# Kernel tuning notes

Hardware: AMD Instinct MI355X
Metric: run time of the kernel (lower is better)

Reference implementation:

```python
import jax, jax.numpy as jnp
import numpy as np

B, T, NB, D, E = 2, 4096, 4, 512, 4096
TEMP = 1.0
CAP_F = 1.5
NOISE_KEY = 42


def setup_inputs() -> dict:
    key = jax.random.key(0)
    k1, k2 = jax.random.split(key)
    x = jax.random.normal(k1, (B, T, NB * D), dtype=jnp.float32)
    # Tied weights: embedding_table[i].weight is embedding_decoder[i].weight, shape [E, D] per block
    W = jax.random.normal(k2, (NB, E, D), dtype=jnp.float32) * 0.02
    return {"x": x, "W": W}


def reference(x, W):
    Bv, Tv, _ = x.shape
    xb = x.reshape(Bv, Tv, NB, D)
    expert_capacity = int(Bv * Tv / E * CAP_F)  # = 3 here
    # per-block decoder logits: [B, T, NB, E]
    dist_logits = jnp.einsum('btnd,ned->btne', xb, W)
    # noise = 1 - temperature * rand_like(logits)
    noise = 1.0 - TEMP * jax.random.uniform(jax.random.key(NOISE_KEY), dist_logits.shape, dtype=dist_logits.dtype)
    noisy = dist_logits * noise
    # top-k over the token axis T (dim=1 in torch) per (b, block, element)
    nt = noisy.transpose(0, 2, 3, 1)  # [B, NB, E, T]
    _, topk_idx = jax.lax.top_k(nt, expert_capacity)  # [B, NB, E, k]
    mask = jnp.zeros(nt.shape, dtype=bool)
    bI = jnp.arange(Bv)[:, None, None, None]
    nI = jnp.arange(NB)[None, :, None, None]
    eI = jnp.arange(E)[None, None, :, None]
    mask = mask.at[bI, nI, eI, topk_idx].set(True)
    maskf = mask.transpose(0, 3, 1, 2).astype(noisy.dtype)  # [B, T, NB, E]
    # argmax over codebook dim of masked noisy logits
    decoded_indices = jnp.argmax(maskf * noisy, axis=-1)  # [B, T, NB]
    # embedding gather with tied table W[n]: [B, T, NB, D]
    latents = jax.vmap(lambda w, i: w[i], in_axes=(0, 2), out_axes=2)(W, decoded_indices)
    decoded_latents = latents.reshape(Bv, Tv, NB * D)  # cat along dim=2
    return decoded_indices, decoded_latents, dist_logits
```

## Files before the change

### kernel.cpp

```cpp
#include <hip/hip_runtime.h>
#include <stdint.h>

#define B_     2
#define T_     4096
#define NB_    4
#define D_     512
#define E_     4096
#define NE_    16384
#define HALF_  67108864u
#define SLOTS_ 32768
#define XN8_   2097152
#define WN8_   1048576
#define MT_    32
#define RECN_  (64 * NE_)

typedef unsigned long long u64;
typedef uint32_t u32;
typedef uint16_t u16;
typedef _Float16 f16x8 __attribute__((ext_vector_type(8)));
typedef float    f32x4 __attribute__((ext_vector_type(4)));

__device__ __forceinline__ u32 rotl32(u32 x, int r) { return __builtin_rotateleft32(x, r); }

__device__ __forceinline__ void tf_0_42(u32 x0, u32 x1, u32 &o0, u32 &o1) {
  const u32 ks0 = 0u, ks1 = 42u, ks2 = 0x1BD11BDAu ^ 0u ^ 42u;
  x0 += ks0; x1 += ks1;
#define TFR(r) { x0 += x1; x1 = rotl32(x1, (r)); x1 ^= x0; }
  TFR(13) TFR(15) TFR(26) TFR(6)
  x0 += ks1; x1 += ks2 + 1u;
  TFR(17) TFR(29) TFR(16) TFR(24)
  x0 += ks2; x1 += ks0 + 2u;
  TFR(13) TFR(15) TFR(26) TFR(6)
  x0 += ks0; x1 += ks1 + 3u;
  TFR(17) TFR(29) TFR(16) TFR(24)
  x0 += ks1; x1 += ks2 + 4u;
  TFR(13) TFR(15) TFR(26) TFR(6)
  x0 += ks2; x1 += ks0 + 5u;
#undef TFR
  o0 = x0; o1 = x1;
}

__device__ __forceinline__ float noise_at(u32 i) {
  u32 o0, o1; tf_0_42(0u, i, o0, o1);
  u32 bits = o0 ^ o1;
  float f = __uint_as_float((bits >> 9) | 0x3F800000u);
  return 2.0f - f;
}

__device__ __forceinline__ u32 map_f32(float v) {
  u32 u = __float_as_uint(v);
  u32 s = (u32)((int)u >> 31);
  return u ^ (s | 0x80000000u);
}

__device__ __forceinline__ void merge3(u64 &a0, u64 &a1, u64 &a2,
                                       u64 b0, u64 b1, u64 b2) {
  u64 o0, o1, o2;
  if (a0 >= b0) {
    o0 = a0;
    if (a1 >= b0) { o1 = a1; o2 = (a2 >= b0) ? a2 : b0; }
    else          { o1 = b0; o2 = (a1 >= b1) ? a1 : b1; }
  } else {
    o0 = b0;
    if (b1 >= a0) { o1 = b1; o2 = (b2 >= a0) ? b2 : a0; }
    else          { o1 = a0; o2 = (b1 >= a1) ? b1 : a1; }
  }
  a0 = o0; a1 = o1; a2 = o2;
}

#define BASE_KEY 0x80000000FFFFFFFFull
#define SCALE_   2048.0f
#define INV_SC   (1.0f / 4194304.0f)

__global__ __launch_bounds__(256) void init_keys(u64* __restrict__ keys,
                                                 u32* __restrict__ thr) {
  int i = blockIdx.x * 256 + threadIdx.x;
  keys[i] = BASE_KEY;
  thr[i]  = 0u;
}

__device__ __forceinline__ void split8v(const float4 a0, const float4 a1, f16x8 &hi, f16x8 &lo) {
  float fv[8] = {a0.x, a0.y, a0.z, a0.w, a1.x, a1.y, a1.z, a1.w};
#pragma unroll
  for (int j = 0; j < 8; ++j) {
    float f = fv[j] * SCALE_;
    _Float16 h = (_Float16)f;
    hi[j] = h;
    lo[j] = (_Float16)(f - (float)h);
  }
}

__global__ __launch_bounds__(256) void presplit(const float* __restrict__ x,
                                                const float* __restrict__ W,
                                                f16x8* __restrict__ xh, f16x8* __restrict__ xl,
                                                f16x8* __restrict__ wh, f16x8* __restrict__ wl) {
  size_t g = (size_t)blockIdx.x * 256 + threadIdx.x;
  const float4* src;
  f16x8 *dh, *dl;
  size_t off;
  if (g < XN8_) { src = (const float4*)x; dh = xh; dl = xl; off = g; }
  else          { src = (const float4*)W; dh = wh; dl = wl; off = g - XN8_; }
  float4 a0 = src[off * 2], a1 = src[off * 2 + 1];
  f16x8 hi, lo;
  split8v(a0, a1, hi, lo);
  dh[off] = hi; dl[off] = lo;
}

#define BM 128
#define BN 128

__global__ __launch_bounds__(256) void gemm_presample(const f16x8* __restrict__ xh,
                                                      const f16x8* __restrict__ xl,
                                                      const f16x8* __restrict__ wh,
                                                      const f16x8* __restrict__ wl,
                                                      u32* __restrict__ thrbuf) {
  __shared__ f16x8 lds_raw[2048];
  f16x8* AhV = lds_raw;
  f16x8* AlV = lds_raw + 512;
  f16x8* BhV = lds_raw + 1024;
  f16x8* BlV = lds_raw + 1536;

  const int id = blockIdx.x;
  const int e0 = (id & 31) * BN;
  const int n  = (id >> 5) & 3;
  const int b  = id >> 7;

  const int tid  = threadIdx.x;
  const int lane = tid & 63;
  const int wid  = tid >> 6;
  const int wr   = wid >> 1;
  const int wc   = wid & 1;
  const int lm   = lane & 15;
  const int lk   = lane >> 4;

  f32x4 acc[4][4];
#pragma unroll
  for (int i = 0; i < 4; ++i)
#pragma unroll
    for (int j = 0; j < 4; ++j) acc[i][j] = (f32x4){0.f, 0.f, 0.f, 0.f};

  for (int k0 = 0; k0 < D_ / 8; k0 += 4) {
#pragma unroll
    for (int l = 0; l < 2; ++l) {
      int aid = tid + l * 256;
      int r   = aid >> 2;
      int ko  = aid & 3;
      int ps  = ko ^ ((r >> 1) & 3);
      size_t gA = ((size_t)(b * T_ + 32 * r) * NB_ + n) * (D_ / 8) + k0 + ko;
      AhV[r * 4 + ps] = xh[gA];
      AlV[r * 4 + ps] = xl[gA];
      size_t gB = ((size_t)n * E_ + e0 + r) * (D_ / 8) + k0 + ko;
      BhV[r * 4 + ps] = wh[gB];
      BlV[r * 4 + ps] = wl[gB];
    }
    __syncthreads();

    f16x8 bh[4], bl[4];
#pragma unroll
    for (int fn = 0; fn < 4; ++fn) {
      int row = wc * 64 + fn * 16 + lm;
      int ps  = lk ^ ((row >> 1) & 3);
      bh[fn] = BhV[row * 4 + ps];
      bl[fn] = BlV[row * 4 + ps];
    }
#pragma unroll
    for (int fm = 0; fm < 4; ++fm) {
      int row = wr * 64 + fm * 16 + lm;
      int ps  = lk ^ ((row >> 1) & 3);
      f16x8 ah = AhV[row * 4 + ps];
      f16x8 al = AlV[row * 4 + ps];
#pragma unroll
      for (int fn = 0; fn < 4; ++fn) {
        acc[fm][fn] = __builtin_amdgcn_mfma_f32_16x16x32_f16(ah, bh[fn], acc[fm][fn], 0, 0, 0);
        acc[fm][fn] = __builtin_amdgcn_mfma_f32_16x16x32_f16(ah, bl[fn], acc[fm][fn], 0, 0, 0);
        acc[fm][fn] = __builtin_amdgcn_mfma_f32_16x16x32_f16(al, bh[fn], acc[fm][fn], 0, 0, 0);
      }
    }
    __syncthreads();
  }
  u64* ldsK = (u64*)lds_raw;

#pragma unroll
  for (int fn = 0; fn < 4; ++fn) {
    const int e  = e0 + wc * 64 + fn * 16 + lm;
    const int ne = n * E_ + e;
    u32 v0 = 0, v1 = 0, v2 = 0;
    u32 tt0 = 0, tt1 = 0, tt2 = 0;
    const u32 ibase = (u32)b * HALF_ + (u32)ne;
#pragma unroll
    for (int fm = 0; fm < 4; ++fm) {
#pragma unroll
      for (int r = 0; r < 4; ++r) {
        const u32 t = 32u * (u32)(wr * 64 + fm * 16 + lk * 4 + r);
        float lg = acc[fm][fn][r] * INV_SC;
        u32 mu = __float_as_uint(fmaxf(lg, 0.0f)) | 0x80000000u;
        if (mu > v2) {
          float y = lg * noise_at(ibase + t * (u32)NE_);
          u32 mv = map_f32(y);
          bool g0 = mv > v0, g1 = mv > v1, g2 = mv > v2;
          v2  = g1 ? v1  : (g2 ? mv : v2);
          tt2 = g1 ? tt1 : (g2 ? t  : tt2);
          v1  = g0 ? v0  : (g1 ? mv : v1);
          tt1 = g0 ? tt0 : (g1 ? t  : tt1);
          v0  = g0 ? mv  : v0;
          tt0 = g0 ? t   : tt0;
        }
      }
    }
    u64 K0 = ((u64)v0 << 32) | (u64)(0xFFFFFFFFu - tt0);
    u64 K1 = ((u64)v1 << 32) | (u64)(0xFFFFFFFFu - tt1);
    u64 K2 = ((u64)v2 << 32) | (u64)(0xFFFFFFFFu - tt2);
    u64 p0 = __shfl_xor(K0, 16), p1 = __shfl_xor(K1, 16), p2 = __shfl_xor(K2, 16);
    merge3(K0, K1, K2, p0, p1, p2);
    p0 = __shfl_xor(K0, 32); p1 = __shfl_xor(K1, 32); p2 = __shfl_xor(K2, 32);
    merge3(K0, K1, K2, p0, p1, p2);
    if (lk == 0) {
      int c = fn * 16 + lm;
      ldsK[(wid * 64 + c) * 3 + 0] = K0;
      ldsK[(wid * 64 + c) * 3 + 1] = K1;
      ldsK[(wid * 64 + c) * 3 + 2] = K2;
    }
  }
  __syncthreads();
  if (wid < 2) {
    int c = lane;
    u64 A0 = ldsK[(wid * 64 + c) * 3 + 0];
    u64 A1 = ldsK[(wid * 64 + c) * 3 + 1];
    u64 A2 = ldsK[(wid * 64 + c) * 3 + 2];
    merge3(A0, A1, A2,
           ldsK[((wid + 2) * 64 + c) * 3 + 0],
           ldsK[((wid + 2) * 64 + c) * 3 + 1],
           ldsK[((wid + 2) * 64 + c) * 3 + 2]);
    int eg = e0 + wid * 64 + c;
    thrbuf[(size_t)b * NE_ + (size_t)n * E_ + eg] = (u32)(A2 >> 32);
  }
}

__global__ __launch_bounds__(256) void gemm_fused(const f16x8* __restrict__ xh,
                                                  const f16x8* __restrict__ xl,
                                                  const f16x8* __restrict__ wh,
                                                  const f16x8* __restrict__ wl,
                                                  float* __restrict__ logits,
                                                  u64* __restrict__ k0g,
                                                  u64* __restrict__ k1g,
                                                  u64* __restrict__ k2g,
                                                  u32* __restrict__ thrbuf) {
  __shared__ f16x8 lds_raw[2048];
  f16x8* AhV = lds_raw;
  f16x8* AlV = lds_raw + 512;
  f16x8* BhV = lds_raw + 1024;
  f16x8* BlV = lds_raw + 1536;

  const int id = blockIdx.x;
  const int e0 = (id & 31) * BN;
  const int mt = (id >> 5) & 63;
  const int n  = id >> 11;
  const int m0 = mt * BM;

  const int tid  = threadIdx.x;
  const int lane = tid & 63;
  const int wid  = tid >> 6;
  const int wr   = wid >> 1;
  const int wc   = wid & 1;
  const int lm   = lane & 15;
  const int lk   = lane >> 4;

  f32x4 acc[4][4];
#pragma unroll
  for (int i = 0; i < 4; ++i)
#pragma unroll
    for (int j = 0; j < 4; ++j) acc[i][j] = (f32x4){0.f, 0.f, 0.f, 0.f};

  for (int k0 = 0; k0 < D_ / 8; k0 += 4) {
#pragma unroll
    for (int l = 0; l < 2; ++l) {
      int aid = tid + l * 256;
      int r   = aid >> 2;
      int ko  = aid & 3;
      int ps  = ko ^ ((r >> 1) & 3);
      size_t gA = ((size_t)(m0 + r) * NB_ + n) * (D_ / 8) + k0 + ko;
      AhV[r * 4 + ps] = xh[gA];
      AlV[r * 4 + ps] = xl[gA];
      size_t gB = ((size_t)n * E_ + e0 + r) * (D_ / 8) + k0 + ko;
      BhV[r * 4 + ps] = wh[gB];
      BlV[r * 4 + ps] = wl[gB];
    }
    __syncthreads();

    f16x8 bh[4], bl[4];
#pragma unroll
    for (int fn = 0; fn < 4; ++fn) {
      int row = wc * 64 + fn * 16 + lm;
      int ps  = lk ^ ((row >> 1) & 3);
      bh[fn] = BhV[row * 4 + ps];
      bl[fn] = BlV[row * 4 + ps];
    }
#pragma unroll
    for (int fm = 0; fm < 4; ++fm) {
      int row = wr * 64 + fm * 16 + lm;
      int ps  = lk ^ ((row >> 1) & 3);
      f16x8 ah = AhV[row * 4 + ps];
      f16x8 al = AlV[row * 4 + ps];
#pragma unroll
      for (int fn = 0; fn < 4; ++fn) {
        acc[fm][fn] = __builtin_amdgcn_mfma_f32_16x16x32_f16(ah, bh[fn], acc[fm][fn], 0, 0, 0);
        acc[fm][fn] = __builtin_amdgcn_mfma_f32_16x16x32_f16(ah, bl[fn], acc[fm][fn], 0, 0, 0);
        acc[fm][fn] = __builtin_amdgcn_mfma_f32_16x16x32_f16(al, bh[fn], acc[fm][fn], 0, 0, 0);
      }
    }
    __syncthreads();
  }
  float* lgbuf = (float*)lds_raw;
  u16*   tbuf  = (u16*)((char*)lds_raw + 16384);
  u64*   ldsK  = (u64*)((char*)lds_raw + 24576);

  const int b     = m0 >> 12;
  const int mbase = m0 & (T_ - 1);
  const int mtile = mbase >> 7;

#pragma unroll
  for (int fm = 0; fm < 4; ++fm) {
#pragma unroll
    for (int r = 0; r < 4; ++r) {
      int m = m0 + wr * 64 + fm * 16 + lk * 4 + r;
      float* row = logits + ((size_t)m * NB_ + n) * E_ + e0 + wc * 64 + lm;
#pragma unroll
      for (int fn = 0; fn < 4; ++fn) row[fn * 16] = acc[fm][fn][r] * INV_SC;
    }
  }

#pragma unroll
  for (int fn = 0; fn < 4; ++fn) {
    const int e  = e0 + wc * 64 + fn * 16 + lm;
    const int ne = n * E_ + e;
    const u32 thrv = thrbuf[(size_t)b * NE_ + ne];

    int cnt = 0;
#pragma unroll
    for (int fm = 0; fm < 4; ++fm) {
#pragma unroll
      for (int r = 0; r < 4; ++r) {
        float lg = acc[fm][fn][r] * INV_SC;
        u32 mu = __float_as_uint(fmaxf(lg, 0.0f)) | 0x80000000u;
        if (mu >= thrv) {
          lgbuf[cnt * 256 + tid] = lg;
          tbuf [cnt * 256 + tid] = (u16)(mbase + wr * 64 + fm * 16 + lk * 4 + r);
          ++cnt;
        }
      }
    }

    u32 v0 = 0, v1 = 0, v2 = 0;
    u32 tt0 = 0, tt1 = 0, tt2 = 0;
    const u32 ibase = (u32)b * HALF_ + (u32)ne;
    for (int k = 0; k < cnt; ++k) {
      float lg = lgbuf[k * 256 + tid];
      u32 t    = (u32)tbuf[k * 256 + tid];
      float y  = lg * noise_at(ibase + t * (u32)NE_);
      u32 mv = map_f32(y);
      bool g0 = mv > v0, g1 = mv > v1, g2 = mv > v2;
      v2  = g1 ? v1  : (g2 ? mv : v2);
      tt2 = g1 ? tt1 : (g2 ? t  : tt2);
      v1  = g0 ? v0  : (g1 ? mv : v1);
      tt1 = g0 ? tt0 : (g1 ? t  : tt1);
      v0  = g0 ? mv  : v0;
      tt0 = g0 ? t   : tt0;
    }

    u64 K0 = ((u64)v0 << 32) | (u64)(0xFFFFFFFFu - tt0);
    u64 K1 = ((u64)v1 << 32) | (u64)(0xFFFFFFFFu - tt1);
    u64 K2 = ((u64)v2 << 32) | (u64)(0xFFFFFFFFu - tt2);
    u64 p0 = __shfl_xor(K0, 16), p1 = __shfl_xor(K1, 16), p2 = __shfl_xor(K2, 16);
    merge3(K0, K1, K2, p0, p1, p2);
    p0 = __shfl_xor(K0, 32); p1 = __shfl_xor(K1, 32); p2 = __shfl_xor(K2, 32);
    merge3(K0, K1, K2, p0, p1, p2);
    if (lk == 0) {
      int c = fn * 16 + lm;
      ldsK[(wid * 64 + c) * 3 + 0] = K0;
      ldsK[(wid * 64 + c) * 3 + 1] = K1;
      ldsK[(wid * 64 + c) * 3 + 2] = K2;
    }
  }
  __syncthreads();
  if (wid < 2) {
    int c = lane;
    u64 A0 = ldsK[(wid * 64 + c) * 3 + 0];
    u64 A1 = ldsK[(wid * 64 + c) * 3 + 1];
    u64 A2 = ldsK[(wid * 64 + c) * 3 + 2];
    u64 C0 = ldsK[((wid + 2) * 64 + c) * 3 + 0];
    u64 C1 = ldsK[((wid + 2) * 64 + c) * 3 + 1];
    u64 C2 = ldsK[((wid + 2) * 64 + c) * 3 + 2];
    merge3(A0, A1, A2, C0, C1, C2);
    int eg = e0 + wid * 64 + c;
    size_t R = (size_t)(mtile * 2 + b) * NE_ + (size_t)n * E_ + eg;
    k0g[R] = A0; k1g[R] = A1; k2g[R] = A2;
    atomicMax(&thrbuf[(size_t)b * NE_ + (size_t)n * E_ + eg], (u32)(A2 >> 32));
  }
}

__global__ __launch_bounds__(256) void merge_scatter2(const u64* __restrict__ k0g,
                                                      const u64* __restrict__ k1g,
                                                      const u64* __restrict__ k2g,
                                                      u64* __restrict__ keys) {
  int gid2 = blockIdx.x * 256 + threadIdx.x;
  int b  = gid2 >> 14;
  int ne = gid2 & (NE_ - 1);

  u64 K0 = 0, K1 = 0, K2 = 0;
  for (int mt = 0; mt < MT_; ++mt) {
    size_t R = (size_t)(mt * 2 + b) * NE_ + ne;
    merge3(K0, K1, K2, k0g[R], k1g[R], k2g[R]);
  }

  int n = ne >> 12;
  u32 e = (u32)(ne & (E_ - 1));
  u64 elo = (u64)(0xFFFFFFFFu - e);
  u32 t0 = 0xFFFFFFFFu - (u32)K0;
  u32 t1 = 0xFFFFFFFFu - (u32)K1;
  u32 t2 = 0xFFFFFFFFu - (u32)K2;
  atomicMax(&keys[((size_t)b * T_ + t0) * NB_ + n], (K0 & 0xFFFFFFFF00000000ull) | elo);
  atomicMax(&keys[((size_t)b * T_ + t1) * NB_ + n], (K1 & 0xFFFFFFFF00000000ull) | elo);
  atomicMax(&keys[((size_t)b * T_ + t2) * NB_ + n], (K2 & 0xFFFFFFFF00000000ull) | elo);
}

__device__ __forceinline__ void split8(const float* __restrict__ p, f16x8 &hi, f16x8 &lo) {
  float4 a0 = *(const float4*)p;
  float4 a1 = *(const float4*)(p + 4);
  split8v(a0, a1, hi, lo);
}

__global__ __launch_bounds__(256) void gemm_logits_fb(const float* __restrict__ x,
                                                      const float* __restrict__ W,
                                                      float* __restrict__ logits) {
  __shared__ f16x8 AhV[128 * 4];
  __shared__ f16x8 AlV[128 * 4];
  __shared__ f16x8 BhV[128 * 4];
  __shared__ f16x8 BlV[128 * 4];

  const int n  = blockIdx.z;
  const int m0 = blockIdx.y * BM;
  const int e0 = blockIdx.x * BN;
  const int tid  = threadIdx.x;
  const int lane = tid & 63;
  const int wid  = tid >> 6;
  const int wr   = wid >> 1;
  const int wc   = wid & 1;
  const int lm   = lane & 15;
  const int lk   = lane >> 4;

  const float* Abase = x + ((size_t)m0 * NB_ + n) * D_;
  const float* Bbase = W + ((size_t)n * E_ + e0) * D_;

  f32x4 acc[4][4];
#pragma unroll
  for (int i = 0; i < 4; ++i)
#pragma unroll
    for (int j = 0; j < 4; ++j) acc[i][j] = (f32x4){0.f, 0.f, 0.f, 0.f};

  for (int k0 = 0; k0 < D_; k0 += 32) {
#pragma unroll
    for (int l = 0; l < 2; ++l) {
      int aid = tid + l * 256;
      int r   = aid >> 2;
      int ko  = aid & 3;
      int ps  = ko ^ ((r >> 1) & 3);
      f16x8 hi, lo;
      split8(Abase + (size_t)r * (NB_ * D_) + k0 + ko * 8, hi, lo);
      AhV[r * 4 + ps] = hi; AlV[r * 4 + ps] = lo;
      split8(Bbase + (size_t)r * D_ + k0 + ko * 8, hi, lo);
      BhV[r * 4 + ps] = hi; BlV[r * 4 + ps] = lo;
    }
    __syncthreads();

    f16x8 bh[4], bl[4];
#pragma unroll
    for (int fn = 0; fn < 4; ++fn) {
      int row = wc * 64 + fn * 16 + lm;
      int ps  = lk ^ ((row >> 1) & 3);
      bh[fn] = BhV[row * 4 + ps];
      bl[fn] = BlV[row * 4 + ps];
    }
#pragma unroll
    for (int fm = 0; fm < 4; ++fm) {
      int row = wr * 64 + fm * 16 + lm;
      int ps  = lk ^ ((row >> 1) & 3);
      f16x8 ah = AhV[row * 4 + ps];
      f16x8 al = AlV[row * 4 + ps];
#pragma unroll
      for (int fn = 0; fn < 4; ++fn) {
        acc[fm][fn] = __builtin_amdgcn_mfma_f32_16x16x32_f16(ah, bh[fn], acc[fm][fn], 0, 0, 0);
        acc[fm][fn] = __builtin_amdgcn_mfma_f32_16x16x32_f16(ah, bl[fn], acc[fm][fn], 0, 0, 0);
        acc[fm][fn] = __builtin_amdgcn_mfma_f32_16x16x32_f16(al, bh[fn], acc[fm][fn], 0, 0, 0);
      }
    }
    __syncthreads();
  }

#pragma unroll
  for (int fm = 0; fm < 4; ++fm) {
#pragma unroll
    for (int fn = 0; fn < 4; ++fn) {
#pragma unroll
      for (int r = 0; r < 4; ++r) {
        int m = m0 + wr * 64 + fm * 16 + lk * 4 + r;
        int e = e0 + wc * 64 + fn * 16 + lm;
        logits[((size_t)m * NB_ + n) * E_ + e] = acc[fm][fn][r] * INV_SC;
      }
    }
  }
}

__global__ __launch_bounds__(256) void select_scatter(const float* __restrict__ logits,
                                                      u64* __restrict__ keys) {
  int gid = blockIdx.x * 256 + threadIdx.x;
  int b  = gid >> 14;
  int ne = gid & (NE_ - 1);

  float v0 = -1e30f, v1 = -1e30f, v2 = -1e30f;
  int   t0 = 0, t1 = 0, t2 = 0;

  const float* lg = logits + (size_t)b * HALF_;
  const u32 ib = (u32)b * HALF_ + (u32)ne;
  for (int t = 0; t < T_; ++t) {
    u32 i0 = (u32)t * (u32)NE_ + (u32)ne;
    float y = lg[i0] * noise_at(ib + (u32)t * (u32)NE_);
    if (y > v0)      { v2=v1; t2=t1; v1=v0; t1=t0; v0=y; t0=t; }
    else if (y > v1) { v2=v1; t2=t1; v1=y;  t1=t; }
    else if (y > v2) { v2=y;  t2=t; }
  }

  int n = ne >> 12;
  int e = ne & (E_ - 1);
  u64 klo = 0xFFFFFFFFull - (u32)e;
  atomicMax(&keys[((size_t)b * T_ + t0) * NB_ + n], ((u64)map_f32(v0) << 32) | klo);
  atomicMax(&keys[((size_t)b * T_ + t1) * NB_ + n], ((u64)map_f32(v1) << 32) | klo);
  atomicMax(&keys[((size_t)b * T_ + t2) * NB_ + n], ((u64)map_f32(v2) << 32) | klo);
}

__global__ __launch_bounds__(128) void finalize(const u64* __restrict__ keys,
                                                const float* __restrict__ W,
                                                float* __restrict__ out_idx,
                                                float* __restrict__ out_lat) {
  int slot = blockIdx.x;
  int n = slot & (NB_ - 1);
  int e = (int)(0xFFFFFFFFu - (u32)keys[slot]) & (E_ - 1);
  if (threadIdx.x == 0) out_idx[slot] = (float)e;

  const float4 v = ((const float4*)(W + ((size_t)n * E_ + e) * D_))[threadIdx.x];
  ((float4*)(out_lat + (size_t)slot * D_))[threadIdx.x] = v;
}

extern "C" void kernel_launch(void* const* d_in, const int* in_sizes, int n_in,
                              void* d_out, int out_size, void* d_ws, size_t ws_size,
                              hipStream_t stream) {
  const float* x = (const float*)d_in[0];
  const float* W = (const float*)d_in[1];

  float* out_idx    = (float*)d_out;
  float* out_lat    = out_idx + (size_t)SLOTS_;
  float* out_logits = out_lat + (size_t)SLOTS_ * D_;

  u64* keys = (u64*)d_ws;
  const size_t KEYS_B = (size_t)SLOTS_ * 8;
  const size_t THR_B  = (size_t)SLOTS_ * 4;
  const size_t XH_B   = (size_t)XN8_ * 16;
  const size_t WH_B   = (size_t)WN8_ * 16;
  bool split = ws_size >= KEYS_B + THR_B + 2 * XH_B + 2 * WH_B;

  u32*   thr = (u32*)((char*)d_ws + KEYS_B);
  char*  sp  = (char*)d_ws + KEYS_B + THR_B;
  f16x8* xh  = (f16x8*)sp;
  f16x8* xl  = (f16x8*)(sp + XH_B);
  f16x8* wh  = (f16x8*)(sp + 2 * XH_B);
  f16x8* wl  = (f16x8*)(sp + 2 * XH_B + WH_B);

  u64* k0g = (u64*)out_lat;
  u64* k1g = k0g + RECN_;
  u64* k2g = k1g + RECN_;

  init_keys<<<SLOTS_ / 256, 256, 0, stream>>>(keys, thr);

  if (split) {
    presplit<<<(XN8_ + WN8_) / 256, 256, 0, stream>>>(x, W, xh, xl, wh, wl);
    gemm_presample<<<256, 256, 0, stream>>>(xh, xl, wh, wl, thr);
    gemm_fused<<<8192, 256, 0, stream>>>(xh, xl, wh, wl, out_logits, k0g, k1g, k2g, thr);
    merge_scatter2<<<SLOTS_ / 256, 256, 0, stream>>>(k0g, k1g, k2g, keys);
  } else {
    dim3 ggrid(E_ / BN, (B_ * T_) / BM, NB_);
    gemm_logits_fb<<<ggrid, 256, 0, stream>>>(x, W, out_logits);
    select_scatter<<<SLOTS_ / 256, 256, 0, stream>>>(out_logits, keys);
  }

  finalize<<<SLOTS_, 128, 0, stream>>>(keys, W, out_idx, out_lat);
}
```

Before: 710.1 us.

## Double-buffer fused GEMM tiles with direct global-to-LDS async loads

The main fused GEMM kernel now stages operand tiles straight from global memory into LDS using the global_load_lds builtin, and ping-pongs between two LDS buffers so the next K-slice loads while MFMAs run on the current one. The aim is to hide global load latency and drop the register round-trip of the old load-then-store staging. The price is double the LDS footprint, which may lower occupancy. The swizzle is now applied to the global source offset rather than the LDS destination, so correctness depends on the builtin's per-lane write layout matching the compute-side reads. The other two kernels only get the compute loop factored into a shared helper.

```diff
diff --git a/kernel.cpp b/kernel.cpp
--- a/kernel.cpp
+++ b/kernel.cpp
@@ -19,6 +19,10 @@
 typedef uint16_t u16;
 typedef _Float16 f16x8 __attribute__((ext_vector_type(8)));
 typedef float    f32x4 __attribute__((ext_vector_type(4)));
+
+#define GLD(srcp, dstp) __builtin_amdgcn_global_load_lds( \
+    (const __attribute__((address_space(1))) void*)(srcp), \
+    (__attribute__((address_space(3))) void*)(dstp), 16, 0, 0)
 
 __device__ __forceinline__ u32 rotl32(u32 x, int r) { return __builtin_rotateleft32(x, r); }
 
@@ -109,6 +113,56 @@
 #define BM 128
 #define BN 128
 
+__device__ __forceinline__ void stage_tile(const f16x8* __restrict__ xh,
+                                           const f16x8* __restrict__ xl,
+                                           const f16x8* __restrict__ wh,
+                                           const f16x8* __restrict__ wl,
+                                           f16x8* buf, int m0, int n, int e0,
+                                           int k0, int w, int lane) {
+#pragma unroll
+  for (int i = 0; i < 2; ++i) {
+    int sbase = w * 128 + i * 64;
+    int s  = sbase + lane;
+    int r  = s >> 2;
+    int ko = (s & 3) ^ ((r >> 1) & 3);
+    size_t gA = ((size_t)(m0 + r) * NB_ + n) * (D_ / 8) + k0 + ko;
+    size_t gB = ((size_t)n * E_ + e0 + r) * (D_ / 8) + k0 + ko;
+    GLD(xh + gA, buf + sbase);
+    GLD(xl + gA, buf + 512 + sbase);
+    GLD(wh + gB, buf + 1024 + sbase);
+    GLD(wl + gB, buf + 1536 + sbase);
+  }
+}
+
+__device__ __forceinline__ void compute_step(const f16x8* buf, f32x4 acc[4][4],
+                                             int wr, int wc, int lm, int lk) {
+  const f16x8* Ah = buf;
+  const f16x8* Al = buf + 512;
+  const f16x8* Bh = buf + 1024;
+  const f16x8* Bl = buf + 1536;
+  f16x8 bh[4], bl[4];
+#pragma unroll
+  for (int fn = 0; fn < 4; ++fn) {
+    int row = wc * 64 + fn * 16 + lm;
+    int ps  = lk ^ ((row >> 1) & 3);
+    bh[fn] = Bh[row * 4 + ps];
+    bl[fn] = Bl[row * 4 + ps];
+  }
+#pragma unroll
+  for (int fm = 0; fm < 4; ++fm) {
+    int row = wr * 64 + fm * 16 + lm;
+    int ps  = lk ^ ((row >> 1) & 3);
+    f16x8 ah = Ah[row * 4 + ps];
+    f16x8 al = Al[row * 4 + ps];
+#pragma unroll
+    for (int fn = 0; fn < 4; ++fn) {
+      acc[fm][fn] = __builtin_amdgcn_mfma_f32_16x16x32_f16(ah, bh[fn], acc[fm][fn], 0, 0, 0);
+      acc[fm][fn] = __builtin_amdgcn_mfma_f32_16x16x32_f16(ah, bl[fn], acc[fm][fn], 0, 0, 0);
+      acc[fm][fn] = __builtin_amdgcn_mfma_f32_16x16x32_f16(al, bh[fn], acc[fm][fn], 0, 0, 0);
+    }
+  }
+}
+
 __global__ __launch_bounds__(256) void gemm_presample(const f16x8* __restrict__ xh,
                                                       const f16x8* __restrict__ xl,
                                                       const f16x8* __restrict__ wh,
@@ -154,28 +208,7 @@
       BlV[r * 4 + ps] = wl[gB];
     }
     __syncthreads();
-
-    f16x8 bh[4], bl[4];
-#pragma unroll
-    for (int fn = 0; fn < 4; ++fn) {
-      int row = wc * 64 + fn * 16 + lm;
-      int ps  = lk ^ ((row >> 1) & 3);
-      bh[fn] = BhV[row * 4 + ps];
-      bl[fn] = BlV[row * 4 + ps];
-    }
-#pragma unroll
-    for (int fm = 0; fm < 4; ++fm) {
-      int row = wr * 64 + fm * 16 + lm;
-      int ps  = lk ^ ((row >> 1) & 3);
-      f16x8 ah = AhV[row * 4 + ps];
-      f16x8 al = AlV[row * 4 + ps];
-#pragma unroll
-      for (int fn = 0; fn < 4; ++fn) {
-        acc[fm][fn] = __builtin_amdgcn_mfma_f32_16x16x32_f16(ah, bh[fn], acc[fm][fn], 0, 0, 0);
-        acc[fm][fn] = __builtin_amdgcn_mfma_f32_16x16x32_f16(ah, bl[fn], acc[fm][fn], 0, 0, 0);
-        acc[fm][fn] = __builtin_amdgcn_mfma_f32_16x16x32_f16(al, bh[fn], acc[fm][fn], 0, 0, 0);
-      }
-    }
+    compute_step(lds_raw, acc, wr, wc, lm, lk);
     __syncthreads();
   }
   u64* ldsK = (u64*)lds_raw;
@@ -245,11 +278,9 @@
                                                   u64* __restrict__ k1g,
                                                   u64* __restrict__ k2g,
                                                   u32* __restrict__ thrbuf) {
-  __shared__ f16x8 lds_raw[2048];
-  f16x8* AhV = lds_raw;
-  f16x8* AlV = lds_raw + 512;
-  f16x8* BhV = lds_raw + 1024;
-  f16x8* BlV = lds_raw + 1536;
+  __shared__ f16x8 lds_raw[4096];
+  f16x8* bufA = lds_raw;
+  f16x8* bufB = lds_raw + 2048;
 
   const int id = blockIdx.x;
   const int e0 = (id & 31) * BN;
@@ -271,45 +302,18 @@
 #pragma unroll
     for (int j = 0; j < 4; ++j) acc[i][j] = (f32x4){0.f, 0.f, 0.f, 0.f};
 
-  for (int k0 = 0; k0 < D_ / 8; k0 += 4) {
-#pragma unroll
-    for (int l = 0; l < 2; ++l) {
-      int aid = tid + l * 256;
-      int r   = aid >> 2;
-      int ko  = aid & 3;
-      int ps  = ko ^ ((r >> 1) & 3);
-      size_t gA = ((size_t)(m0 + r) * NB_ + n) * (D_ / 8) + k0 + ko;
-      AhV[r * 4 + ps] = xh[gA];
-      AlV[r * 4 + ps] = xl[gA];
-      size_t gB = ((size_t)n * E_ + e0 + r) * (D_ / 8) + k0 + ko;
-      BhV[r * 4 + ps] = wh[gB];
-      BlV[r * 4 + ps] = wl[gB];
-    }
+  stage_tile(xh, xl, wh, wl, bufA, m0, n, e0, 0, wid, lane);
+  __syncthreads();
+  for (int kk = 0; kk < 16; kk += 2) {
+    stage_tile(xh, xl, wh, wl, bufB, m0, n, e0, 4 * (kk + 1), wid, lane);
+    compute_step(bufA, acc, wr, wc, lm, lk);
     __syncthreads();
-
-    f16x8 bh[4], bl[4];
-#pragma unroll
-    for (int fn = 0; fn < 4; ++fn) {
-      int row = wc * 64 + fn * 16 + lm;
-      int ps  = lk ^ ((row >> 1) & 3);
-      bh[fn] = BhV[row * 4 + ps];
-      bl[fn] = BlV[row * 4 + ps];
-    }
-#pragma unroll
-    for (int fm = 0; fm < 4; ++fm) {
-      int row = wr * 64 + fm * 16 + lm;
-      int ps  = lk ^ ((row >> 1) & 3);
-      f16x8 ah = AhV[row * 4 + ps];
-      f16x8 al = AlV[row * 4 + ps];
-#pragma unroll
-      for (int fn = 0; fn < 4; ++fn) {
-        acc[fm][fn] = __builtin_amdgcn_mfma_f32_16x16x32_f16(ah, bh[fn], acc[fm][fn], 0, 0, 0);
-        acc[fm][fn] = __builtin_amdgcn_mfma_f32_16x16x32_f16(ah, bl[fn], acc[fm][fn], 0, 0, 0);
-        acc[fm][fn] = __builtin_amdgcn_mfma_f32_16x16x32_f16(al, bh[fn], acc[fm][fn], 0, 0, 0);
-      }
-    }
+    if (kk < 14)
+      stage_tile(xh, xl, wh, wl, bufA, m0, n, e0, 4 * (kk + 2), wid, lane);
+    compute_step(bufB, acc, wr, wc, lm, lk);
     __syncthreads();
   }
+
   float* lgbuf = (float*)lds_raw;
   u16*   tbuf  = (u16*)((char*)lds_raw + 16384);
   u64*   ldsK  = (u64*)((char*)lds_raw + 24576);
@@ -432,10 +436,11 @@
 __global__ __launch_bounds__(256) void gemm_logits_fb(const float* __restrict__ x,
                                                       const float* __restrict__ W,
                                                       float* __restrict__ logits) {
-  __shared__ f16x8 AhV[128 * 4];
-  __shared__ f16x8 AlV[128 * 4];
-  __shared__ f16x8 BhV[128 * 4];
-  __shared__ f16x8 BlV[128 * 4];
+  __shared__ f16x8 lds_raw[2048];
+  f16x8* AhV = lds_raw;
+  f16x8* AlV = lds_raw + 512;
+  f16x8* BhV = lds_raw + 1024;
+  f16x8* BlV = lds_raw + 1536;
 
   const int n  = blockIdx.z;
   const int m0 = blockIdx.y * BM;
@@ -471,28 +476,7 @@
       BhV[r * 4 + ps] = hi; BlV[r * 4 + ps] = lo;
     }
     __syncthreads();
-
-    f16x8 bh[4], bl[4];
-#pragma unroll
-    for (int fn = 0; fn < 4; ++fn) {
-      int row = wc * 64 + fn * 16 + lm;
-      int ps  = lk ^ ((row >> 1) & 3);
-      bh[fn] = BhV[row * 4 + ps];
-      bl[fn] = BlV[row * 4 + ps];
-    }
-#pragma unroll
-    for (int fm = 0; fm < 4; ++fm) {
-      int row = wr * 64 + fm * 16 + lm;
-      int ps  = lk ^ ((row >> 1) & 3);
-      f16x8 ah = AhV[row * 4 + ps];
-      f16x8 al = AlV[row * 4 + ps];
-#pragma unroll
-      for (int fn = 0; fn < 4; ++fn) {
-        acc[fm][fn] = __builtin_amdgcn_mfma_f32_16x16x32_f16(ah, bh[fn], acc[fm][fn], 0, 0, 0);
-        acc[fm][fn] = __builtin_amdgcn_mfma_f32_16x16x32_f16(ah, bl[fn], acc[fm][fn], 0, 0, 0);
-        acc[fm][fn] = __builtin_amdgcn_mfma_f32_16x16x32_f16(al, bh[fn], acc[fm][fn], 0, 0, 0);
-      }
-    }
+    compute_step(lds_raw, acc, wr, wc, lm, lk);
     __syncthreads();
   }
 
```

Result: faster. 680.8 us (-4.1%).
